# Kernel tuning notes

Hardware: AMD Instinct MI355X
Metric: run time of the kernel (lower is better)

## Reference

```python
import jax, jax.numpy as jnp
import numpy as np

N = 100000      # nodes
E = 1600000     # edges (avg degree 16)
D = 128         # input feature dim
UNITS = 64      # ChebyNet units
K = 3           # Chebyshev order
C = 40          # num_classes
LMAX = 2.0      # lambda_max for rw-normalized Laplacian


def setup_inputs() -> dict:
    key = jax.random.key(0)
    ks = jax.random.split(key, 6)
    x = jax.random.normal(ks[0], (N, D), dtype=jnp.float32)
    edge_index = jax.random.randint(ks[1], (2, E), 0, N, dtype=jnp.int32)
    edge_weight = jax.random.uniform(ks[2], (E,), dtype=jnp.float32)
    W = jax.random.normal(ks[3], (K, D, UNITS), dtype=jnp.float32) * 0.05   # per-order Cheb kernels
    b = jnp.zeros((UNITS,), dtype=jnp.float32)
    Wd = jax.random.normal(ks[4], (UNITS, C), dtype=jnp.float32) * 0.05     # final Dense
    bd = jnp.zeros((C,), dtype=jnp.float32)
    return {"x": x, "edge_index": edge_index, "edge_weight": edge_weight,
            "W": W, "b": b, "Wd": Wd, "bd": bd}


def reference(x, edge_index, edge_weight, W, b, Wd, bd):
    src, dst = edge_index[0], edge_index[1]
    # rw normalization: A_hat = D^{-1} A, deg computed at dst
    deg = jax.ops.segment_sum(edge_weight, dst, num_segments=N)
    w_norm = edge_weight / jnp.maximum(deg[dst], 1e-12)  # [E]

    def lhat(h):
        # L h = h - D^{-1} A h ; L_hat = (2/lmax) L - I
        ah = jax.ops.segment_sum(h[src] * w_norm[:, None], dst, num_segments=N)  # [N, D]
        return (2.0 / LMAX) * (h - ah) - h

    # Chebyshev recursion T_0 = x, T_1 = L_hat x, T_2 = 2 L_hat T_1 - T_0
    T0 = x
    T1 = lhat(T0)
    T2 = 2.0 * lhat(T1) - T0
    h = T0 @ W[0] + T1 @ W[1] + T2 @ W[2] + b  # [N, UNITS]
    return h @ Wd + bd                          # [N, C]
```

## Files before the change

kernel.cpp:

```cpp
#include <hip/hip_runtime.h>

namespace {
constexpr int N = 100000;
constexpr int E = 1600000;
constexpr int D = 128;
constexpr int U = 64;
constexpr int C = 40;
constexpr int C2 = C / 2;
constexpr int RP = 32;
constexpr int SLOTS = 64;
constexpr int NB = (N + 255) / 256;
constexpr int CAP = 4608;
constexpr int EPB = 16;
constexpr int TPB = 256;
constexpr int GK = 136;

constexpr size_t OFF_BCUR = 0;
constexpr size_t OFF_META = OFF_BCUR + 512;
constexpr size_t OFF_CSR = OFF_META + (size_t)2 * N;
constexpr size_t OFF_BBUF = OFF_CSR + (size_t)2 * N * SLOTS;
constexpr size_t OFF_P1 = OFF_BBUF;
constexpr size_t OFF_P2B = OFF_P1 + (size_t)N * C + 32;
constexpr size_t BBUF_INTS = (size_t)NB * CAP * 4;
constexpr size_t PROJ_INTS = (size_t)N * C + 32 + (size_t)N * RP;
constexpr size_t REGION = BBUF_INTS > PROJ_INTS ? BBUF_INTS : PROJ_INTS;
constexpr size_t OFF_RBF = OFF_BBUF + REGION;
constexpr size_t OFF_GBF = OFF_RBF + (size_t)N * RP;
constexpr size_t OFF_BC = OFF_GBF + 128 * GK / 2;
}

__device__ inline unsigned f2bf(float x) {
    unsigned u = __float_as_uint(x);
    return (u + 0x7fffu + ((u >> 16) & 1u)) >> 16;
}
__device__ inline unsigned pack_bf2(float a, float b) { return f2bf(a) | (f2bf(b) << 16); }
__device__ inline float2 unpack_bf2(unsigned v) {
    return make_float2(__uint_as_float(v << 16), __uint_as_float(v & 0xffff0000u));
}

__global__ void prep_weights(const float* __restrict__ W, const float* __restrict__ b,
                             const float* __restrict__ Wd, const float* __restrict__ bd,
                             unsigned short* __restrict__ Gbf, float* __restrict__ bc) {
    int t = blockIdx.x * blockDim.x + threadIdx.x;
    if (t < 128 * 128) {
        int n = t >> 7, k = t & 127;
        float s = 0.f;
        if (n < 40) {
            const float* W0 = W + (size_t)k * U;
            const float* W2 = W + (size_t)2 * D * U + (size_t)k * U;
            for (int u = 0; u < U; ++u) s += (W0[u] - W2[u]) * Wd[u * C + n];
        } else if (n < 80) {
            const float* W1 = W + (size_t)D * U + (size_t)k * U;
            for (int u = 0; u < U; ++u) s -= W1[u] * Wd[u * C + (n - 40)];
        } else if (n < 120) {
            const float* W2 = W + (size_t)2 * D * U + (size_t)k * U;
            for (int u = 0; u < U; ++u) s += 2.f * W2[u] * Wd[u * C + (n - 80)];
        }
        Gbf[n * GK + k] = (unsigned short)f2bf(s);
    } else if (t < 128 * 128 + C) {
        int c = t - 128 * 128;
        float s = bd[c];
        for (int u = 0; u < U; ++u) s += b[u] * Wd[u * C + c];
        bc[c] = s;
    }
}

__global__ __launch_bounds__(TPB) void bucket_scatter(const int* __restrict__ src,
                                                      const int* __restrict__ dst,
                                                      const float* __restrict__ ew,
                                                      int* __restrict__ bcur,
                                                      int4* __restrict__ bbuf) {
    __shared__ int hist[NB];
    __shared__ int base[NB];
    int t = threadIdx.x;
    for (int i = t; i < NB; i += TPB) hist[i] = 0;
    __syncthreads();

    size_t e0 = (size_t)blockIdx.x * (TPB * EPB);
    int ms[EPB], md[EPB], mw[EPB], mr[EPB];
#pragma unroll
    for (int k = 0; k < EPB; ++k) {
        size_t e = e0 + (size_t)k * TPB + t;
        if (e < E) {
            ms[k] = src[e];
            md[k] = dst[e];
            mw[k] = __float_as_int(ew[e]);
            mr[k] = atomicAdd(&hist[md[k] >> 8], 1);
        } else {
            md[k] = -1;
        }
    }
    __syncthreads();
    for (int i = t; i < NB; i += TPB) {
        int c = hist[i];
        base[i] = c ? atomicAdd(&bcur[i], c) : 0;
    }
    __syncthreads();
#pragma unroll
    for (int k = 0; k < EPB; ++k) {
        if (md[k] >= 0) {
            int bkt = md[k] >> 8;
            int slot = base[bkt] + mr[k];
            if (slot < CAP) bbuf[(size_t)bkt * CAP + slot] = make_int4(ms[k], mw[k], md[k], 0);
        }
    }
}

__global__ __launch_bounds__(256) void csr_build(const int* __restrict__ bcur,
                                                 const int4* __restrict__ bbuf,
                                                 int2* __restrict__ meta,
                                                 int2* __restrict__ csr) {
    __shared__ int lcur[256];
    __shared__ float lw[256];
    int b = blockIdx.x;
    int t = threadIdx.x;
    lcur[t] = 0;
    lw[t] = 0.f;
    __syncthreads();
    int cnt = min(bcur[b], CAP);
    for (int i = t; i < cnt; i += 256) {
        int4 r = bbuf[(size_t)b * CAP + i];
        int idx = r.z & 255;
        int slot = atomicAdd(&lcur[idx], 1);
        atomicAdd(&lw[idx], __int_as_float(r.y));
        if (slot < SLOTS) csr[((size_t)r.z << 6) + slot] = make_int2(r.x, r.y);
    }
    __syncthreads();
    int node = (b << 8) + t;
    if (node < N) {
        int c = min(lcur[t], SLOTS);
        float rdeg = 1.f / fmaxf(lw[t], 1e-12f);
        meta[node] = make_int2(c, __float_as_int(rdeg));
        int padded = min((c + 15) & ~15, SLOTS);
        for (int s = c; s < padded; ++s)
            csr[((size_t)node << 6) + s] = make_int2(0, 0);
    }
}

typedef __attribute__((ext_vector_type(8))) short bf16x8;
typedef __attribute__((ext_vector_type(4))) float f32x4;

__global__ __launch_bounds__(256) void proj_mfma(const float* __restrict__ X,
                                                 const unsigned* __restrict__ Gu,
                                                 const float* __restrict__ bc,
                                                 float* __restrict__ out,
                                                 float* __restrict__ P1,
                                                 unsigned short* __restrict__ P2B16) {
    __shared__ __align__(16) unsigned short a_s[64 * GK];
    __shared__ __align__(16) unsigned short g_s[128 * GK];
    __shared__ float bc_s[C];
    int t = threadIdx.x;
    int rb = blockIdx.x;

    unsigned* gsu = (unsigned*)g_s;
    for (int i = t; i < 128 * GK / 2; i += 256) gsu[i] = Gu[i];
    if (t < C) bc_s[t] = bc[t];

#pragma unroll
    for (int i = 0; i < 8; ++i) {
        int idx = i * 256 + t;
        int row = idx >> 5, kq = idx & 31;
        size_t grow = (size_t)rb * 64 + row;
        float4 v = (grow < N) ? ((const float4*)X)[grow * 32 + kq]
                              : make_float4(0.f, 0.f, 0.f, 0.f);
        unsigned* dstp = (unsigned*)(a_s + row * GK + kq * 4);
        dstp[0] = pack_bf2(v.x, v.y);
        dstp[1] = pack_bf2(v.z, v.w);
    }
    __syncthreads();

    int w = t >> 6, l = t & 63;
    int lr = l & 15, lh = l >> 4;

    bf16x8 afr[4];
#pragma unroll
    for (int ks = 0; ks < 4; ++ks)
        afr[ks] = *(const bf16x8*)(a_s + (w * 16 + lr) * GK + ks * 32 + lh * 8);

    f32x4 acc[8];
#pragma unroll
    for (int tt = 0; tt < 8; ++tt) {
        acc[tt] = (f32x4){0.f, 0.f, 0.f, 0.f};
#pragma unroll
        for (int ks = 0; ks < 4; ++ks) {
            bf16x8 bfr = *(const bf16x8*)(g_s + (tt * 16 + lr) * GK + ks * 32 + lh * 8);
            acc[tt] = __builtin_amdgcn_mfma_f32_16x16x32_bf16(afr[ks], bfr, acc[tt], 0, 0, 0);
        }
    }

#pragma unroll
    for (int tt = 0; tt < 8; ++tt) {
        int gcol = tt * 16 + lr;
#pragma unroll
        for (int r = 0; r < 4; ++r) {
            size_t grow = (size_t)rb * 64 + w * 16 + lh * 4 + r;
            if (grow >= N) continue;
            float v = acc[tt][r];
            if (gcol < 40) {
                out[grow * C + gcol] = v + bc_s[gcol];
            } else if (gcol < 80) {
                P1[grow * C + (gcol - 40)] = v;
            } else if (gcol < 120) {
                P2B16[grow * 64 + (gcol - 80)] = (unsigned short)f2bf(v);
            }
        }
    }
}

template <bool OUT_BF>
__global__ __launch_bounds__(256) void spmm40v4(const int2* __restrict__ meta,
                                                const int2* __restrict__ csr,
                                                const unsigned* __restrict__ Xg,
                                                const float* __restrict__ Add,
                                                void* __restrict__ Yv) {
    int wid = (blockIdx.x * blockDim.x + threadIdx.x) >> 6;
    if (wid >= N) return;
    int uw = __builtin_amdgcn_readfirstlane(wid);
    int2 m = meta[uw];
    int c = m.x;
    float rdeg = __int_as_float(m.y);
    const int2* __restrict__ row = csr + ((size_t)uw << 6);
    int lane = threadIdx.x & 63;
    bool hi = lane >= 32;
    unsigned voff = (unsigned)(lane & 31);

    float2 ad = make_float2(0.f, 0.f);
    if (lane < C2) ad = ((const float2*)Add)[(size_t)wid * C2 + lane];

    float2 acc = make_float2(0.f, 0.f);
    for (int j0 = 0; j0 < c; j0 += 16) {
        unsigned va[8];
        float wa[8];
#pragma unroll
        for (int k = 0; k < 8; ++k) {
            int2 a = row[j0 + k];
            int2 b = row[j0 + 8 + k];
            int col = hi ? b.x : a.x;
            wa[k] = __int_as_float(hi ? b.y : a.y);
            va[k] = Xg[((unsigned)col << 5) + voff];
        }
#pragma unroll
        for (int k = 0; k < 8; ++k) {
            float2 v = unpack_bf2(va[k]);
            acc.x = fmaf(wa[k], v.x, acc.x);
            acc.y = fmaf(wa[k], v.y, acc.y);
        }
    }
    acc.x += __shfl_xor(acc.x, 32);
    acc.y += __shfl_xor(acc.y, 32);

    if (OUT_BF) {
        if (lane < 32) {
            unsigned o = 0u;
            if (lane < C2)
                o = pack_bf2(fmaf(acc.x, rdeg, ad.x), fmaf(acc.y, rdeg, ad.y));
            ((unsigned*)Yv)[((size_t)wid << 5) + lane] = o;
        }
    } else {
        if (lane < C2) {
            ((float2*)Yv)[(size_t)wid * C2 + lane] =
                make_float2(fmaf(acc.x, rdeg, ad.x), fmaf(acc.y, rdeg, ad.y));
        }
    }
}

extern "C" void kernel_launch(void* const* d_in, const int* in_sizes, int n_in,
                              void* d_out, int out_size, void* d_ws, size_t ws_size,
                              hipStream_t stream) {
    const float* x = (const float*)d_in[0];
    const int* ei = (const int*)d_in[1];
    const float* ew = (const float*)d_in[2];
    const float* W = (const float*)d_in[3];
    const float* b = (const float*)d_in[4];
    const float* Wd = (const float*)d_in[5];
    const float* bd = (const float*)d_in[6];
    float* out = (float*)d_out;

    const int* src = ei;
    const int* dst = ei + E;

    float* ws = (float*)d_ws;
    int* bcur = (int*)(ws + OFF_BCUR);
    int2* meta = (int2*)(ws + OFF_META);
    int2* csr = (int2*)(ws + OFF_CSR);
    int4* bbuf = (int4*)(ws + OFF_BBUF);
    float* P1 = ws + OFF_P1;
    unsigned* P2B = (unsigned*)(ws + OFF_P2B);
    unsigned* Rbf = (unsigned*)(ws + OFF_RBF);
    unsigned short* Gbf = (unsigned short*)(ws + OFF_GBF);
    float* bc = ws + OFF_BC;

    hipMemsetAsync((char*)d_ws + OFF_BCUR * sizeof(int), 0, 512 * sizeof(int), stream);

    prep_weights<<<(128 * 128 + C + 255) / 256, 256, 0, stream>>>(W, b, Wd, bd, Gbf, bc);

    bucket_scatter<<<(E + TPB * EPB - 1) / (TPB * EPB), TPB, 0, stream>>>(src, dst, ew, bcur, bbuf);
    csr_build<<<NB, 256, 0, stream>>>(bcur, bbuf, meta, csr);

    proj_mfma<<<(N + 63) / 64, 256, 0, stream>>>(x, (const unsigned*)Gbf, bc, out, P1,
                                                 (unsigned short*)P2B);

    spmm40v4<true><<<((size_t)N * 64 + 255) / 256, 256, 0, stream>>>(meta, csr, P2B, P1, Rbf);
    spmm40v4<false><<<((size_t)N * 64 + 255) / 256, 256, 0, stream>>>(meta, csr, Rbf, out, out);
}
```

Measured before the change: 150.2 us.

## Merge CSR build with projection kernel, shrink bucket records, fold memset into prep

The memset of the bucket counters moves into prep_weights, so one launch goes away. Bucket records shrink from int4 to int2 by packing the low 8 bits of the destination into the top byte of the source index. csr_build and proj_mfma become one launch: the first NB blocks build the CSR and the rest run the projection, so the two can overlap. This requires non-overlapping buffers, so the workspace layout is changed to give the bucket buffer and projection outputs separate regions. The packing assumes source indices fit in 24 bits, and every block of the merged kernel now reserves the projection's larger shared-memory footprint, which may lower occupancy for the CSR blocks.

```diff
diff --git a/kernel.cpp b/kernel.cpp
--- a/kernel.cpp
+++ b/kernel.cpp
@@ -14,19 +14,20 @@
 constexpr int EPB = 16;
 constexpr int TPB = 256;
 constexpr int GK = 136;
+constexpr int PROJ_BLOCKS = (N + 63) / 64;
 
 constexpr size_t OFF_BCUR = 0;
 constexpr size_t OFF_META = OFF_BCUR + 512;
 constexpr size_t OFF_CSR = OFF_META + (size_t)2 * N;
 constexpr size_t OFF_BBUF = OFF_CSR + (size_t)2 * N * SLOTS;
-constexpr size_t OFF_P1 = OFF_BBUF;
+constexpr size_t BBUF_INTS = (size_t)NB * CAP * 2;
+constexpr size_t OFF_P1 = OFF_BBUF + BBUF_INTS;
 constexpr size_t OFF_P2B = OFF_P1 + (size_t)N * C + 32;
-constexpr size_t BBUF_INTS = (size_t)NB * CAP * 4;
-constexpr size_t PROJ_INTS = (size_t)N * C + 32 + (size_t)N * RP;
-constexpr size_t REGION = BBUF_INTS > PROJ_INTS ? BBUF_INTS : PROJ_INTS;
-constexpr size_t OFF_RBF = OFF_BBUF + REGION;
+constexpr size_t OFF_RBF = OFF_P2B + (size_t)N * RP;
 constexpr size_t OFF_GBF = OFF_RBF + (size_t)N * RP;
 constexpr size_t OFF_BC = OFF_GBF + 128 * GK / 2;
+
+constexpr int SMEM_PROJ = 64 * GK * 2 + 128 * GK * 2 + ((C * 4 + 15) & ~15);
 }
 
 __device__ inline unsigned f2bf(float x) {
@@ -38,9 +39,16 @@
     return make_float2(__uint_as_float(v << 16), __uint_as_float(v & 0xffff0000u));
 }
 
+typedef __attribute__((ext_vector_type(8))) short bf16x8;
+typedef __attribute__((ext_vector_type(4))) float f32x4;
+
 __global__ void prep_weights(const float* __restrict__ W, const float* __restrict__ b,
                              const float* __restrict__ Wd, const float* __restrict__ bd,
-                             unsigned short* __restrict__ Gbf, float* __restrict__ bc) {
+                             unsigned short* __restrict__ Gbf, float* __restrict__ bc,
+                             int* __restrict__ bcur) {
+    if (blockIdx.x == 0) {
+        for (int i = threadIdx.x; i < 512; i += 256) bcur[i] = 0;
+    }
     int t = blockIdx.x * blockDim.x + threadIdx.x;
     if (t < 128 * 128) {
         int n = t >> 7, k = t & 127;
@@ -69,7 +77,7 @@
                                                       const int* __restrict__ dst,
                                                       const float* __restrict__ ew,
                                                       int* __restrict__ bcur,
-                                                      int4* __restrict__ bbuf) {
+                                                      int2* __restrict__ bbuf2) {
     __shared__ int hist[NB];
     __shared__ int base[NB];
     int t = threadIdx.x;
@@ -101,56 +109,56 @@
         if (md[k] >= 0) {
             int bkt = md[k] >> 8;
             int slot = base[bkt] + mr[k];
-            if (slot < CAP) bbuf[(size_t)bkt * CAP + slot] = make_int4(ms[k], mw[k], md[k], 0);
-        }
-    }
-}
-
-__global__ __launch_bounds__(256) void csr_build(const int* __restrict__ bcur,
-                                                 const int4* __restrict__ bbuf,
-                                                 int2* __restrict__ meta,
-                                                 int2* __restrict__ csr) {
-    __shared__ int lcur[256];
-    __shared__ float lw[256];
-    int b = blockIdx.x;
+            if (slot < CAP)
+                bbuf2[(size_t)bkt * CAP + slot] =
+                    make_int2(ms[k] | ((md[k] & 255) << 24), mw[k]);
+        }
+    }
+}
+
+__global__ __launch_bounds__(256) void csr_and_proj(
+    const int* __restrict__ bcur, const int2* __restrict__ bbuf2,
+    int2* __restrict__ meta, int2* __restrict__ csr,
+    const float* __restrict__ X, const unsigned* __restrict__ Gu,
+    const float* __restrict__ bc, float* __restrict__ out,
+    float* __restrict__ P1, unsigned short* __restrict__ P2B16) {
+    __shared__ __align__(16) unsigned char smem[SMEM_PROJ];
     int t = threadIdx.x;
-    lcur[t] = 0;
-    lw[t] = 0.f;
-    __syncthreads();
-    int cnt = min(bcur[b], CAP);
-    for (int i = t; i < cnt; i += 256) {
-        int4 r = bbuf[(size_t)b * CAP + i];
-        int idx = r.z & 255;
-        int slot = atomicAdd(&lcur[idx], 1);
-        atomicAdd(&lw[idx], __int_as_float(r.y));
-        if (slot < SLOTS) csr[((size_t)r.z << 6) + slot] = make_int2(r.x, r.y);
-    }
-    __syncthreads();
-    int node = (b << 8) + t;
-    if (node < N) {
-        int c = min(lcur[t], SLOTS);
-        float rdeg = 1.f / fmaxf(lw[t], 1e-12f);
-        meta[node] = make_int2(c, __float_as_int(rdeg));
-        int padded = min((c + 15) & ~15, SLOTS);
-        for (int s = c; s < padded; ++s)
-            csr[((size_t)node << 6) + s] = make_int2(0, 0);
-    }
-}
-
-typedef __attribute__((ext_vector_type(8))) short bf16x8;
-typedef __attribute__((ext_vector_type(4))) float f32x4;
-
-__global__ __launch_bounds__(256) void proj_mfma(const float* __restrict__ X,
-                                                 const unsigned* __restrict__ Gu,
-                                                 const float* __restrict__ bc,
-                                                 float* __restrict__ out,
-                                                 float* __restrict__ P1,
-                                                 unsigned short* __restrict__ P2B16) {
-    __shared__ __align__(16) unsigned short a_s[64 * GK];
-    __shared__ __align__(16) unsigned short g_s[128 * GK];
-    __shared__ float bc_s[C];
-    int t = threadIdx.x;
-    int rb = blockIdx.x;
+
+    if (blockIdx.x < NB) {
+        int* lcur = (int*)smem;
+        float* lw = (float*)(smem + 1024);
+        int b = blockIdx.x;
+        lcur[t] = 0;
+        lw[t] = 0.f;
+        __syncthreads();
+        int cnt = min(bcur[b], CAP);
+        for (int i = t; i < cnt; i += 256) {
+            int2 r = bbuf2[(size_t)b * CAP + i];
+            int idx = ((unsigned)r.x) >> 24;
+            int srcn = r.x & 0x00FFFFFF;
+            int slot = atomicAdd(&lcur[idx], 1);
+            atomicAdd(&lw[idx], __int_as_float(r.y));
+            if (slot < SLOTS)
+                csr[(((size_t)(b << 8) + idx) << 6) + slot] = make_int2(srcn, r.y);
+        }
+        __syncthreads();
+        int node = (b << 8) + t;
+        if (node < N) {
+            int c = min(lcur[t], SLOTS);
+            float rdeg = 1.f / fmaxf(lw[t], 1e-12f);
+            meta[node] = make_int2(c, __float_as_int(rdeg));
+            int padded = min((c + 15) & ~15, SLOTS);
+            for (int s = c; s < padded; ++s)
+                csr[((size_t)node << 6) + s] = make_int2(0, 0);
+        }
+        return;
+    }
+
+    int rb = blockIdx.x - NB;
+    unsigned short* a_s = (unsigned short*)smem;
+    unsigned short* g_s = (unsigned short*)(smem + 64 * GK * 2);
+    float* bc_s = (float*)(smem + 64 * GK * 2 + 128 * GK * 2);
 
     unsigned* gsu = (unsigned*)g_s;
     for (int i = t; i < 128 * GK / 2; i += 256) gsu[i] = Gu[i];
@@ -283,22 +291,20 @@
     int* bcur = (int*)(ws + OFF_BCUR);
     int2* meta = (int2*)(ws + OFF_META);
     int2* csr = (int2*)(ws + OFF_CSR);
-    int4* bbuf = (int4*)(ws + OFF_BBUF);
+    int2* bbuf2 = (int2*)(ws + OFF_BBUF);
     float* P1 = ws + OFF_P1;
     unsigned* P2B = (unsigned*)(ws + OFF_P2B);
     unsigned* Rbf = (unsigned*)(ws + OFF_RBF);
     unsigned short* Gbf = (unsigned short*)(ws + OFF_GBF);
     float* bc = ws + OFF_BC;
 
-    hipMemsetAsync((char*)d_ws + OFF_BCUR * sizeof(int), 0, 512 * sizeof(int), stream);
-
-    prep_weights<<<(128 * 128 + C + 255) / 256, 256, 0, stream>>>(W, b, Wd, bd, Gbf, bc);
-
-    bucket_scatter<<<(E + TPB * EPB - 1) / (TPB * EPB), TPB, 0, stream>>>(src, dst, ew, bcur, bbuf);
-    csr_build<<<NB, 256, 0, stream>>>(bcur, bbuf, meta, csr);
-
-    proj_mfma<<<(N + 63) / 64, 256, 0, stream>>>(x, (const unsigned*)Gbf, bc, out, P1,
-                                                 (unsigned short*)P2B);
+    prep_weights<<<(128 * 128 + C + 255) / 256, 256, 0, stream>>>(W, b, Wd, bd, Gbf, bc, bcur);
+
+    bucket_scatter<<<(E + TPB * EPB - 1) / (TPB * EPB), TPB, 0, stream>>>(src, dst, ew, bcur, bbuf2);
+
+    csr_and_proj<<<NB + PROJ_BLOCKS, 256, 0, stream>>>(bcur, bbuf2, meta, csr, x,
+                                                       (const unsigned*)Gbf, bc, out, P1,
+                                                       (unsigned short*)P2B);
 
     spmm40v4<true><<<((size_t)N * 64 + 255) / 256, 256, 0, stream>>>(meta, csr, P2B, P1, Rbf);
     spmm40v4<false><<<((size_t)N * 64 + 255) / 256, 256, 0, stream>>>(meta, csr, Rbf, out, out);
```

After: 131.1 us. 12.7% less time.
